# Optimization experiments

Hardware: AMD Instinct MI355X
Metric: run time of the kernel (lower is better)

The kernel has to match this reference:

```python
import jax, jax.numpy as jnp
import numpy as np

EMB = 2048
N_HEADS = 16
HEAD_DIM = EMB // N_HEADS
ROPE_BASE = 10000.0


def _rope_cos_sin(seq_len, head_dim, dtype):
    inv_freq = 1.0 / (ROPE_BASE ** (jnp.arange(0, head_dim, 2, dtype=jnp.float32) / head_dim))
    t = jnp.arange(seq_len, dtype=jnp.float32)
    freqs = jnp.einsum('s,d->sd', t, inv_freq)          # [S, head_dim/2]
    emb = jnp.concatenate([freqs, freqs], axis=-1)       # [S, head_dim]
    return jnp.cos(emb).astype(dtype), jnp.sin(emb).astype(dtype)


def _rotate_half(x):
    x1, x2 = jnp.split(x, 2, axis=-1)
    return jnp.concatenate([-x2, x1], axis=-1)


def _apply_rope(x, cos, sin):
    # x: [B, H, S, D]; cos/sin: [S, D]
    return x * cos[None, None, :, :] + _rotate_half(x) * sin[None, None, :, :]


def setup_inputs() -> dict:
    key = jax.random.key(0)
    k1, k2, k3 = jax.random.split(key, 3)
    B, S = 4, 2048
    x = jax.random.normal(k1, (B, S, EMB), dtype=jnp.float32)
    # Additive causal mask: 0 on/below diagonal, -1e9 above.
    causal = jnp.triu(jnp.full((S, S), -1e9, dtype=jnp.float32), k=1)
    att_mask = causal[None, None, :, :]
    Wqkv = jax.random.normal(k2, (3 * EMB, EMB), dtype=jnp.float32) * (EMB ** -0.5)
    Wout = jax.random.normal(k3, (EMB, EMB), dtype=jnp.float32) * (EMB ** -0.5)
    return {"x": x, "att_mask": att_mask, "Wqkv": Wqkv, "Wout": Wout}


def reference(x, att_mask, Wqkv, Wout):
    B, S, E = x.shape
    qkv = jnp.einsum('bse,fe->bsf', x, Wqkv)             # [B, S, 3E]
    q, k, v = jnp.split(qkv, 3, axis=-1)
    def to_heads(t):
        return t.reshape(B, S, N_HEADS, HEAD_DIM).transpose(0, 2, 1, 3)  # [B,H,S,D]
    q, k, v = to_heads(q), to_heads(k), to_heads(v)
    cos, sin = _rope_cos_sin(S, HEAD_DIM, x.dtype)
    q = _apply_rope(q, cos, sin)
    k = _apply_rope(k, cos, sin)
    scaling = HEAD_DIM ** -0.5
    dots = jnp.einsum('bhqd,bhkd->bhqk', q, k) * scaling
    dots = dots + att_mask
    attn = jax.nn.softmax(dots, axis=-1)
    out = jnp.einsum('bhqk,bhkd->bhqd', attn, v)         # [B,H,S,D]
    out = out.transpose(0, 2, 1, 3).reshape(B, S, E)
    return jnp.einsum('bse,fe->bsf', out, Wout)
```

## Files before the change

### kernel.cpp

```cpp
#include <hip/hip_runtime.h>
#include <stdint.h>

typedef __attribute__((ext_vector_type(8))) short short8_t;
typedef __attribute__((ext_vector_type(4))) float f32x4;

__device__ __forceinline__ short f2bf(float f) {
  union { float f; uint32_t u; } v; v.f = f;
  uint32_t r = v.u + 0x7FFFu + ((v.u >> 16) & 1u);
  return (short)(r >> 16);
}
__device__ __forceinline__ float bf2f(short s) {
  union { uint32_t u; float f; } v; v.u = ((uint32_t)(uint16_t)s) << 16; return v.f;
}
__device__ __forceinline__ void gld16(const void* g, void* l) {
  __builtin_amdgcn_global_load_lds((const __attribute__((address_space(1))) void*)g,
                                   (__attribute__((address_space(3))) void*)l, 16, 0, 0);
}

__global__ __launch_bounds__(256) void conv_kernel(const float* __restrict__ in,
                                                   short* __restrict__ out, int n4) {
  int i = blockIdx.x * 256 + threadIdx.x;
  const int stride = gridDim.x * 256;
  for (; i < n4; i += stride) {
    float4 v = reinterpret_cast<const float4*>(in)[i];
    short4 o;
    o.x = f2bf(v.x); o.y = f2bf(v.y); o.z = f2bf(v.z); o.w = f2bf(v.w);
    reinterpret_cast<short4*>(out)[i] = o;
  }
}

__device__ __forceinline__ void storeC(float* C, size_t i, float v) { C[i] = v; }
__device__ __forceinline__ void storeC(short* C, size_t i, float v) { C[i] = f2bf(v); }

template <typename OT>
__global__ __launch_bounds__(512, 2) void gemm8p(const short* __restrict__ A,
                                                 const short* __restrict__ B,
                                                 OT* __restrict__ C, int M, int N, int K,
                                                 int nbx) {
  __shared__ __align__(16) short lds[65536];
  const int tid = threadIdx.x, lane = tid & 63, w = tid >> 6;
  const int wr = w >> 2, wc = w & 3;
  const int c = lane & 15, g4 = lane >> 4;
  const int lin = (blockIdx.x & 7) * ((int)gridDim.x >> 3) + ((int)blockIdx.x >> 3);
  const int bx = lin % nbx, by = lin / nbx;
  const size_t m0 = (size_t)by * 256, n0 = (size_t)bx * 256;
  const size_t Kb = (size_t)K * 2;
  const char* Ab = (const char*)A + m0 * Kb;
  const char* Bb = (const char*)B + n0 * Kb;
  const char* aq[2];
  const char* bq[2];
#pragma unroll
  for (int i = 0; i < 2; ++i) {
    const size_t ro = (size_t)((i * 8 + w) * 16 + c) * Kb + g4 * 16;
    aq[i] = Ab + ro;
    bq[i] = Bb + ro;
  }
  char* alds = (char*)lds;
  const int aoff = wr * 8192 + lane * 16;
  const int boff = 65536 + wc * 4096 + lane * 16;
  f32x4 acc[8][4] = {};
  const int NT = K >> 6, NIT = NT >> 1;

  short8_t af[2][4], bfr[2][4];

#define STAGE(q, srcoff, ldsbase)                                  \
  gld16((q)[0] + (srcoff), alds + (ldsbase) + (w << 10));          \
  gld16((q)[1] + (srcoff), alds + (ldsbase) + ((8 + w) << 10))

  STAGE(aq, 0, 0);
  STAGE(bq, 0, 65536);
  STAGE(aq, 64, 16384);
  STAGE(bq, 64, 81920);
  STAGE(aq, 128, 32768);
  STAGE(bq, 128, 98304);
  asm volatile("s_waitcnt vmcnt(0)" ::: "memory");
  asm volatile("s_barrier" ::: "memory");

#define RD_A(S, mi, OFF) \
  asm volatile("ds_read_b128 %0, %1 offset:%c2" : "=v"(af[S][mi]) : "v"(aoff), "i"(OFF))
#define RD_B(S, ni, OFF) \
  asm volatile("ds_read_b128 %0, %1 offset:%c2" : "=v"(bfr[S][ni]) : "v"(boff), "i"(OFF))

#define PREF_A(S, BSEL, KS, MQ)                           \
  RD_A(S, 0, (BSEL) + (KS)*16384 + ((MQ)*4 + 0) * 1024);  \
  RD_A(S, 1, (BSEL) + (KS)*16384 + ((MQ)*4 + 1) * 1024);  \
  RD_A(S, 2, (BSEL) + (KS)*16384 + ((MQ)*4 + 2) * 1024);  \
  RD_A(S, 3, (BSEL) + (KS)*16384 + ((MQ)*4 + 3) * 1024)

#define PREF_B(S, BSEL, KS)                  \
  RD_B(S, 0, (BSEL) + (KS)*16384 + 0);       \
  RD_B(S, 1, (BSEL) + (KS)*16384 + 1024);    \
  RD_B(S, 2, (BSEL) + (KS)*16384 + 2048);    \
  RD_B(S, 3, (BSEL) + (KS)*16384 + 3072)

#define MFMA16(AS, BS, MQ)                                                               \
  __builtin_amdgcn_s_setprio(1);                                                         \
  _Pragma("unroll") for (int mi = 0; mi < 4; ++mi) {                                     \
    _Pragma("unroll") for (int n = 0; n < 4; ++n)                                        \
      acc[(MQ)*4 + mi][n] = __builtin_amdgcn_mfma_f32_16x16x32_bf16(                     \
          af[AS][mi], bfr[BS][n], acc[(MQ)*4 + mi][n], 0, 0, 0);                         \
  }                                                                                      \
  __builtin_amdgcn_s_setprio(0)

#define PHASE_E(AS, BS, PBSEL, PKS, q, srcoff, sbase)              \
  PREF_A(AS ^ 1, PBSEL, PKS, 1);                                   \
  STAGE(q, srcoff, sbase);                                         \
  asm volatile("s_waitcnt lgkmcnt(4)" ::: "memory");               \
  __builtin_amdgcn_sched_barrier(0);                               \
  MFMA16(AS, BS, 0);                                               \
  asm volatile("s_waitcnt vmcnt(6)" ::: "memory");                 \
  asm volatile("s_barrier" ::: "memory")

#define PHASE_O(AS, BS, PBSEL, PKS, q, srcoff, sbase)              \
  PREF_B(BS ^ 1, PBSEL, PKS);                                      \
  PREF_A(AS ^ 1, PBSEL, PKS, 0);                                   \
  STAGE(q, srcoff, sbase);                                         \
  asm volatile("s_waitcnt lgkmcnt(8)" ::: "memory");               \
  __builtin_amdgcn_sched_barrier(0);                               \
  MFMA16(AS, BS, 1);                                               \
  asm volatile("s_waitcnt vmcnt(8)" ::: "memory");                 \
  asm volatile("s_barrier" ::: "memory")

  PREF_B(0, 0, 0);
  PREF_A(0, 0, 0, 0);

  for (int it = 0; it < NIT; ++it) {
    const int T = it << 1;
    const int t1 = (T + 1) << 7;
    const int t2 = (T + 2 < NT ? T + 2 : NT - 1) << 7;
    const int t3 = (T + 3 < NT ? T + 3 : NT - 1) << 7;
    PHASE_E(0, 0, 0, 0,      aq, t1 + 64, 49152);
    PHASE_O(1, 0, 0, 1,      bq, t1 + 64, 114688);
    PHASE_E(0, 1, 0, 1,      aq, t2, 0);
    PHASE_O(1, 1, 32768, 0,  bq, t2, 65536);
    PHASE_E(0, 0, 32768, 0,  aq, t2 + 64, 16384);
    PHASE_O(1, 0, 32768, 1,  bq, t2 + 64, 81920);
    PHASE_E(0, 1, 32768, 1,  aq, t3, 32768);
    PHASE_O(1, 1, 0, 0,      bq, t3, 98304);
  }
#undef PHASE_E
#undef PHASE_O
#undef MFMA16
#undef PREF_A
#undef PREF_B
#undef RD_A
#undef RD_B
#undef STAGE

#pragma unroll
  for (int m = 0; m < 8; ++m)
#pragma unroll
    for (int n = 0; n < 4; ++n) {
      const size_t col = n0 + wc * 64 + n * 16 + c;
      const size_t rb = m0 + wr * 128 + m * 16 + g4 * 4;
#pragma unroll
      for (int r = 0; r < 4; ++r) storeC(C, (rb + r) * (size_t)N + col, acc[m][n][r]);
    }
}

__global__ __launch_bounds__(256) void rope_kernel(short* __restrict__ qkv) {
  const int g = blockIdx.x * 256 + threadIdx.x;
  const int jg = g & 7;
  const int h = (g >> 3) & 15;
  const int bs = g >> 7;
  const int s = bs & 2047;
  const size_t base = (size_t)bs * 6144 + 2048 + h * 128 + jg * 8;
  short8_t lo = *(short8_t*)&qkv[base];
  short8_t hi = *(short8_t*)&qkv[base + 64];
  short8_t olo, ohi;
#pragma unroll
  for (int t = 0; t < 8; ++t) {
    const int j = jg * 8 + t;
    const float inv = exp2f((float)j * -0.20762050593046f);
    float sn, cn;
    sincosf((float)s * inv, &sn, &cn);
    const float a = bf2f(lo[t]), b = bf2f(hi[t]);
    olo[t] = f2bf(a * cn - b * sn);
    ohi[t] = f2bf(b * cn + a * sn);
  }
  *(short8_t*)&qkv[base] = olo;
  *(short8_t*)&qkv[base + 64] = ohi;
}

__global__ __launch_bounds__(256) void vt_kernel(const short* __restrict__ qkv,
                                                 short* __restrict__ vt) {
  __shared__ __align__(16) short Vl[64][128];
  const int g = blockIdx.x;
  const int st = g & 31, bh = g >> 5;
  const int h = bh & 15, b = bh >> 4;
  const int t = threadIdx.x;
  const int s0 = st * 64;
#pragma unroll
  for (int p = 0; p < 4; ++p) {
    const int idx = p * 256 + t;
    const int row = idx >> 4, c16 = idx & 15;
    short8_t v = *(const short8_t*)&qkv[(size_t)(b * 2048 + s0 + row) * 6144 + 4096 + h * 128 + c16 * 8];
    *(short8_t*)&Vl[row][c16 * 8] = v;
  }
  __syncthreads();
  const size_t obase = ((size_t)(b * 16 + h) * 128) * 2048;
#pragma unroll
  for (int i = 0; i < 8; ++i) {
    const int idx = t * 8 + i;
    const int d = idx >> 4, sq = idx & 15;
    short4 o;
    o.x = Vl[sq * 4 + 0][d];
    o.y = Vl[sq * 4 + 1][d];
    o.z = Vl[sq * 4 + 2][d];
    o.w = Vl[sq * 4 + 3][d];
    *(short4*)&vt[obase + (size_t)d * 2048 + s0 + sq * 4] = o;
  }
}

__global__ __launch_bounds__(256) void attn_kernel(const short* __restrict__ qkv,
                                                   const short* __restrict__ vt,
                                                   short* __restrict__ o) {
  __shared__ __align__(16) short Kl[2][64 * 128];
  __shared__ __align__(16) short Vl[2][128 * 64];
  __shared__ __align__(16) short Pl[4][16 * 72];
  const int tid = threadIdx.x, lane = tid & 63, w = tid >> 6;
  const int c = lane & 15, g4 = lane >> 4;
  const int blk = blockIdx.x;
  const int xcd = blk & 7;
  const int l = blk >> 3;
  const int bh = xcd * 8 + (l >> 5);
  const int h = bh & 15, b = bh >> 4;
  const int q0 = (31 - (l & 31)) * 64;
  const int srow = q0 + w * 16 + c;

  short8_t qf[4];
  {
    const size_t qr = ((size_t)b * 2048 + srow) * 6144 + h * 128;
    float fl[4][8];
#pragma unroll
    for (int dc = 0; dc < 4; ++dc) {
      short8_t rawv = *(const short8_t*)&qkv[qr + dc * 32 + g4 * 8];
#pragma unroll
      for (int t = 0; t < 8; ++t) fl[dc][t] = bf2f(rawv[t]);
    }
#pragma unroll
    for (int pd = 0; pd < 2; ++pd)
#pragma unroll
      for (int t = 0; t < 8; ++t) {
        const int j = pd * 32 + g4 * 8 + t;
        const float inv = exp2f((float)j * -0.20762050593046f);
        float sn, cn;
        sincosf((float)srow * inv, &sn, &cn);
        const float a = fl[pd][t], bb = fl[pd + 2][t];
        fl[pd][t] = a * cn - bb * sn;
        fl[pd + 2][t] = bb * cn + a * sn;
      }
#pragma unroll
    for (int dc = 0; dc < 4; ++dc) {
      short8_t q8;
#pragma unroll
      for (int t = 0; t < 8; ++t) q8[t] = f2bf(fl[dc][t]);
      qf[dc] = q8;
    }
  }

  f32x4 acc_o[8] = {};
  float rs[4] = {0.f, 0.f, 0.f, 0.f};
  const float scale2 = 0.12751875222364685f;
  const char* Kbase = (const char*)qkv + ((size_t)b * 2048 * 6144 + 2048 + h * 128) * 2;
  const char* Vbase = (const char*)vt + ((size_t)(b * 16 + h) * 128 * 2048) * 2;

  const char* kq[4];
  const char* vq[4];
#pragma unroll
  for (int i = 0; i < 4; ++i) {
    const int L = ((w * 4 + i) << 10) + lane * 16;
    {
      const int row = L >> 8, inner = L & 255;
      kq[i] = Kbase + (size_t)row * 12288 + (inner ^ ((row & 7) << 4));
    }
    {
      const int row = L >> 7, inner = L & 127;
      vq[i] = Vbase + (size_t)row * 4096 + (inner ^ ((row & 7) << 4));
    }
  }
  auto stage = [&](int buf, int kv0) {
#pragma unroll
    for (int i = 0; i < 4; ++i) {
      gld16(kq[i] + (size_t)kv0 * 12288, (char*)Kl + (buf << 14) + ((w * 4 + i) << 10));
      gld16(vq[i] + (size_t)kv0 * 2, (char*)Vl + (buf << 14) + ((w * 4 + i) << 10));
    }
  };

  stage(0, 0);
  __syncthreads();
  int cur = 0;
  for (int kv0 = 0; kv0 <= q0; kv0 += 64) {
    if (kv0 + 64 <= q0) stage(cur ^ 1, kv0 + 64);
    const char* Kb = (const char*)Kl + (cur << 14);
    const char* Vb = (const char*)Vl + (cur << 14);
    const bool diag = (kv0 == q0);
    float p[4][4];
#pragma unroll
    for (int kt = 0; kt < 4; ++kt) {
      f32x4 s4 = {};
      const int krow = kt * 16 + c;
      __builtin_amdgcn_s_setprio(1);
#pragma unroll
      for (int dc = 0; dc < 4; ++dc) {
        const int inner = (dc * 64 + g4 * 16) ^ ((krow & 7) << 4);
        short8_t kf = *(const short8_t*)(Kb + krow * 256 + inner);
        s4 = __builtin_amdgcn_mfma_f32_16x16x32_bf16(qf[dc], kf, s4, 0, 0, 0);
      }
      __builtin_amdgcn_s_setprio(0);
#pragma unroll
      for (int r = 0; r < 4; ++r) {
        float v = s4[r] * scale2 - 8.0f;
        if (diag) {
          const int kc = kv0 + kt * 16 + c;
          const int qr2 = q0 + w * 16 + g4 * 4 + r;
          if (kc > qr2) v = -1e30f;
        }
        const float pe = exp2f(v);
        p[kt][r] = pe;
        rs[r] += pe;
      }
    }
#pragma unroll
    for (int kt = 0; kt < 4; ++kt)
#pragma unroll
      for (int r = 0; r < 4; r += 2) {
        uint32_t pk;
        asm("v_cvt_pk_bf16_f32 %0, %1, %2" : "=v"(pk) : "v"(p[kt][r]), "v"(p[kt][r + 1]));
        Pl[w][(g4 * 4 + r) * 72 + kt * 16 + c] = (short)(pk & 0xffffu);
        Pl[w][(g4 * 4 + r + 1) * 72 + kt * 16 + c] = (short)(pk >> 16);
      }
#pragma unroll
    for (int kk = 0; kk < 2; ++kk) {
      short8_t pf = *(const short8_t*)&Pl[w][c * 72 + kk * 32 + g4 * 8];
      __builtin_amdgcn_s_setprio(1);
#pragma unroll
      for (int dt = 0; dt < 8; ++dt) {
        const int vrow = dt * 16 + c;
        const int inner = (kk * 64 + g4 * 16) ^ ((vrow & 7) << 4);
        short8_t vf = *(const short8_t*)(Vb + vrow * 128 + inner);
        acc_o[dt] = __builtin_amdgcn_mfma_f32_16x16x32_bf16(pf, vf, acc_o[dt], 0, 0, 0);
      }
      __builtin_amdgcn_s_setprio(0);
    }
    __syncthreads();
    cur ^= 1;
  }
#pragma unroll
  for (int off = 1; off < 16; off <<= 1)
#pragma unroll
    for (int r = 0; r < 4; ++r) rs[r] += __shfl_xor(rs[r], off);
  const size_t ob = ((size_t)b * 2048 + q0 + w * 16 + g4 * 4) * 2048 + h * 128;
#pragma unroll
  for (int dt = 0; dt < 8; ++dt)
#pragma unroll
    for (int r = 0; r < 4; ++r)
      o[ob + (size_t)r * 2048 + dt * 16 + c] = f2bf(acc_o[dt][r] / rs[r]);
}

extern "C" void kernel_launch(void* const* d_in, const int* in_sizes, int n_in,
                              void* d_out, int out_size, void* d_ws, size_t ws_size,
                              hipStream_t stream) {
  const float* x = (const float*)d_in[0];
  const float* Wqkv = (const float*)d_in[2];
  const float* Wout = (const float*)d_in[3];
  float* out = (float*)d_out;
  char* ws = (char*)d_ws;
  short* xb   = (short*)ws;
  short* wqb  = (short*)(ws + 33554432ull);
  short* qkv  = (short*)(ws + 58720256ull);
  short* vt   = (short*)(ws + 159383552ull);
  short* attno = xb;
  short* woutb = wqb;

  conv_kernel<<<2048, 256, 0, stream>>>(x, xb, 16777216 / 4);
  conv_kernel<<<2048, 256, 0, stream>>>(Wqkv, wqb, 12582912 / 4);
  gemm8p<short><<<768, 512, 0, stream>>>(xb, wqb, qkv, 8192, 6144, 2048, 24);
  conv_kernel<<<2048, 256, 0, stream>>>(Wout, woutb, 4194304 / 4);
  rope_kernel<<<4096, 256, 0, stream>>>(qkv);
  vt_kernel<<<2048, 256, 0, stream>>>(qkv, vt);
  attn_kernel<<<2048, 256, 0, stream>>>(qkv, vt, attno);
  gemm8p<float><<<256, 512, 0, stream>>>(attno, woutb, out, 8192, 2048, 2048, 8);
}
```

Measured before the change: 535.9 us.

## Fuse V transpose into QKV GEMM epilogue and remap GEMM tile swizzle

The QKV GEMM epilogue now writes the V columns straight into the transposed [B,H,D,S] buffer as 4-element bf16 stores, so the separate vt_kernel launch and its round trip through global memory go away. The block-to-tile mapping is also replaced with a fixed per-XCD layout: each XCD gets a contiguous band of M tiles and walks N tiles, meant to improve L2 reuse of the A rows. The transposed stores are strided across lanes, so that epilogue write is less coalesced than the original row-major store.

Result: faster. 517.5 us (-3.4%).

```diff
diff --git a/kernel.cpp b/kernel.cpp
--- a/kernel.cpp
+++ b/kernel.cpp
@@ -32,17 +32,20 @@
 __device__ __forceinline__ void storeC(float* C, size_t i, float v) { C[i] = v; }
 __device__ __forceinline__ void storeC(short* C, size_t i, float v) { C[i] = f2bf(v); }
 
-template <typename OT>
+template <typename OT, bool FUSEV>
 __global__ __launch_bounds__(512, 2) void gemm8p(const short* __restrict__ A,
                                                  const short* __restrict__ B,
-                                                 OT* __restrict__ C, int M, int N, int K,
-                                                 int nbx) {
+                                                 OT* __restrict__ C,
+                                                 short* __restrict__ VT,
+                                                 int M, int N, int K) {
   __shared__ __align__(16) short lds[65536];
   const int tid = threadIdx.x, lane = tid & 63, w = tid >> 6;
   const int wr = w >> 2, wc = w & 3;
   const int c = lane & 15, g4 = lane >> 4;
-  const int lin = (blockIdx.x & 7) * ((int)gridDim.x >> 3) + ((int)blockIdx.x >> 3);
-  const int bx = lin % nbx, by = lin / nbx;
+  const int xcd = (int)blockIdx.x & 7;
+  const int t = (int)blockIdx.x >> 3;
+  const int bx = (t & 7) + 8 * (t >> 5);
+  const int by = xcd * 4 + ((t >> 3) & 3);
   const size_t m0 = (size_t)by * 256, n0 = (size_t)bx * 256;
   const size_t Kb = (size_t)K * 2;
   const char* Ab = (const char*)A + m0 * Kb;
@@ -153,8 +156,19 @@
     for (int n = 0; n < 4; ++n) {
       const size_t col = n0 + wc * 64 + n * 16 + c;
       const size_t rb = m0 + wr * 128 + m * 16 + g4 * 4;
-#pragma unroll
-      for (int r = 0; r < 4; ++r) storeC(C, (rb + r) * (size_t)N + col, acc[m][n][r]);
+      bool tovt = false;
+      if constexpr (FUSEV) tovt = (col >= 4096);
+      if (tovt) {
+        const size_t cc = col - 4096;
+        const size_t b = rb >> 11, s0 = rb & 2047;
+        short4 o;
+        o.x = f2bf(acc[m][n][0]); o.y = f2bf(acc[m][n][1]);
+        o.z = f2bf(acc[m][n][2]); o.w = f2bf(acc[m][n][3]);
+        *(short4*)&VT[(b * 2048 + cc) * 2048 + s0] = o;
+      } else {
+#pragma unroll
+        for (int r = 0; r < 4; ++r) storeC(C, (rb + r) * (size_t)N + col, acc[m][n][r]);
+      }
     }
 }
 
@@ -180,36 +194,6 @@
   }
   *(short8_t*)&qkv[base] = olo;
   *(short8_t*)&qkv[base + 64] = ohi;
-}
-
-__global__ __launch_bounds__(256) void vt_kernel(const short* __restrict__ qkv,
-                                                 short* __restrict__ vt) {
-  __shared__ __align__(16) short Vl[64][128];
-  const int g = blockIdx.x;
-  const int st = g & 31, bh = g >> 5;
-  const int h = bh & 15, b = bh >> 4;
-  const int t = threadIdx.x;
-  const int s0 = st * 64;
-#pragma unroll
-  for (int p = 0; p < 4; ++p) {
-    const int idx = p * 256 + t;
-    const int row = idx >> 4, c16 = idx & 15;
-    short8_t v = *(const short8_t*)&qkv[(size_t)(b * 2048 + s0 + row) * 6144 + 4096 + h * 128 + c16 * 8];
-    *(short8_t*)&Vl[row][c16 * 8] = v;
-  }
-  __syncthreads();
-  const size_t obase = ((size_t)(b * 16 + h) * 128) * 2048;
-#pragma unroll
-  for (int i = 0; i < 8; ++i) {
-    const int idx = t * 8 + i;
-    const int d = idx >> 4, sq = idx & 15;
-    short4 o;
-    o.x = Vl[sq * 4 + 0][d];
-    o.y = Vl[sq * 4 + 1][d];
-    o.z = Vl[sq * 4 + 2][d];
-    o.w = Vl[sq * 4 + 3][d];
-    *(short4*)&vt[obase + (size_t)d * 2048 + s0 + sq * 4] = o;
-  }
 }
 
 __global__ __launch_bounds__(256) void attn_kernel(const short* __restrict__ qkv,
@@ -375,10 +359,9 @@
 
   conv_kernel<<<2048, 256, 0, stream>>>(x, xb, 16777216 / 4);
   conv_kernel<<<2048, 256, 0, stream>>>(Wqkv, wqb, 12582912 / 4);
-  gemm8p<short><<<768, 512, 0, stream>>>(xb, wqb, qkv, 8192, 6144, 2048, 24);
+  gemm8p<short, true><<<768, 512, 0, stream>>>(xb, wqb, qkv, vt, 8192, 6144, 2048);
   conv_kernel<<<2048, 256, 0, stream>>>(Wout, woutb, 4194304 / 4);
   rope_kernel<<<4096, 256, 0, stream>>>(qkv);
-  vt_kernel<<<2048, 256, 0, stream>>>(qkv, vt);
   attn_kernel<<<2048, 256, 0, stream>>>(qkv, vt, attno);
-  gemm8p<float><<<256, 512, 0, stream>>>(attno, woutb, out, 8192, 2048, 2048, 8);
-}
+  gemm8p<float, false><<<256, 512, 0, stream>>>(attno, woutb, out, nullptr, 8192, 2048, 2048);
+}
```
